# Performance work log

Measured on AMD Instinct MI355X. Metric: run time of the kernel, lower is better.

Reference implementation:

```python
import jax, jax.numpy as jnp
import numpy as np
import math

W_BITS = 256.0  # default w_bits in forward()

def ste_round(x):
    # straight-through estimator round: identity gradient
    return x + jax.lax.stop_gradient(jnp.round(x) - x)

def setup_inputs() -> dict:
    key = jax.random.key(0)
    k1, k2 = jax.random.split(key)
    x_size, y_size = 4096, 4096
    xb = jax.random.normal(k1, (8192, x_size), dtype=jnp.float32)
    W = jax.random.normal(k2, (x_size, y_size), dtype=jnp.float32) / math.sqrt(x_size)
    b = jnp.zeros((y_size,), dtype=jnp.float32)
    return {"xb": xb, "W": W, "b": b}

def reference(xb, W, b):
    # train=True path: fake-quant the weights (per-tensor symmetric int8), then matmul + bias
    s_w = 2.0 * jnp.max(jnp.abs(W)) / W_BITS          # per-tensor scale (zero-point 0)
    w_q = jnp.clip(ste_round(W / s_w), -127.0, 127.0)  # quantize + clamp
    w_fq = s_w * w_q                                    # dequantize (fake-quant)
    return xb @ w_fq + b
```

## Files before the change

### kernel.cpp

```cpp
#include <hip/hip_runtime.h>
#include <hip/hip_bf16.h>
#include <stdint.h>

typedef unsigned short u16;
typedef unsigned int u32;
typedef __bf16 bf16x8 __attribute__((ext_vector_type(8)));
typedef float f32x4 __attribute__((ext_vector_type(4)));
typedef u16 u16x4 __attribute__((ext_vector_type(4)));

typedef const __attribute__((address_space(1))) void* gas_ptr;
typedef __attribute__((address_space(3))) void* las_ptr;

#define M_DIM 8192
#define K_DIM 4096
#define N_DIM 4096

__device__ __forceinline__ u16 f32_to_bf16_rne(float f) {
    u32 u = __float_as_uint(f);
    u += 0x7FFFu + ((u >> 16) & 1u);
    return (u16)(u >> 16);
}

__global__ void maxabs_kernel(const float* __restrict__ W, u32* __restrict__ out, int n4) {
    int idx = blockIdx.x * blockDim.x + threadIdx.x;
    int stride = gridDim.x * blockDim.x;
    const float4* W4 = (const float4*)W;
    float m = 0.0f;
    for (int i = idx; i < n4; i += stride) {
        float4 v = W4[i];
        m = fmaxf(m, fmaxf(fmaxf(fabsf(v.x), fabsf(v.y)), fmaxf(fabsf(v.z), fabsf(v.w))));
    }
#pragma unroll
    for (int off = 32; off > 0; off >>= 1)
        m = fmaxf(m, __shfl_down(m, off));
    if ((threadIdx.x & 63) == 0)
        atomicMax(out, __float_as_uint(m));
}

__global__ void quant_transpose_kernel(const float* __restrict__ W, u16* __restrict__ Wt,
                                       const u32* __restrict__ mb) {
    __shared__ u16 tile[32][33];
    const float s_inv = 128.0f / __uint_as_float(*mb);
    int n = blockIdx.x * 32 + threadIdx.x;
#pragma unroll
    for (int r = threadIdx.y; r < 32; r += 8) {
        int k = blockIdx.y * 32 + r;
        float q = rintf(W[(size_t)k * N_DIM + n] * s_inv);
        q = fminf(fmaxf(q, -127.0f), 127.0f);
        tile[threadIdx.x][r] = (u16)(__float_as_uint(q) >> 16);
    }
    __syncthreads();
    int k_out = blockIdx.y * 32 + threadIdx.x;
#pragma unroll
    for (int r = threadIdx.y; r < 32; r += 8) {
        int n_out = blockIdx.x * 32 + r;
        Wt[(size_t)n_out * K_DIM + k_out] = tile[r][threadIdx.x];
    }
}

__global__ void cast_bf16_kernel(const float* __restrict__ x, u16* __restrict__ y, int n4) {
    int idx = blockIdx.x * blockDim.x + threadIdx.x;
    int stride = gridDim.x * blockDim.x;
    const float4* x4 = (const float4*)x;
    u16x4* y4 = (u16x4*)y;
    for (int i = idx; i < n4; i += stride) {
        float4 v = x4[i];
        u16x4 o;
        o.x = f32_to_bf16_rne(v.x);
        o.y = f32_to_bf16_rne(v.y);
        o.z = f32_to_bf16_rne(v.z);
        o.w = f32_to_bf16_rne(v.w);
        y4[i] = o;
    }
}


#define BAR() __builtin_amdgcn_s_barrier()
#define LGKM0()                                            \
    do {                                                   \
        asm volatile("s_waitcnt lgkmcnt(0)" ::: "memory"); \
        __builtin_amdgcn_sched_barrier(0);                 \
    } while (0)
#define VMC(N) asm volatile("s_waitcnt vmcnt(" #N ")" ::: "memory")
#define PRIO1() __builtin_amdgcn_s_setprio(1)
#define PRIO0() __builtin_amdgcn_s_setprio(0)

#define DS_A(ABASE, MH)                                            \
    do {                                                           \
        _Pragma("unroll") for (int i_ = 0; i_ < 4; ++i_) {         \
            const char* p_ = (ABASE) + ((MH)*64 + i_ * 16) * 128;  \
            a[i_][0] = *(const bf16x8*)(p_ + ck0);                 \
            a[i_][1] = *(const bf16x8*)(p_ + ck1);                 \
        }                                                          \
    } while (0)

#define DS_B(BBASE, NH)                                            \
    do {                                                           \
        _Pragma("unroll") for (int j_ = 0; j_ < 2; ++j_) {         \
            const char* p_ = (BBASE) + ((NH)*32 + j_ * 16) * 128;  \
            b[(NH)*2 + j_][0] = *(const bf16x8*)(p_ + ck0);        \
            b[(NH)*2 + j_][1] = *(const bf16x8*)(p_ + ck1);        \
        }                                                          \
    } while (0)

#define MM(MH, NH)                                                                            \
    do {                                                                                      \
        _Pragma("unroll") for (int i_ = 0; i_ < 4; ++i_) {                                    \
            _Pragma("unroll") for (int j_ = 0; j_ < 2; ++j_) {                                \
                f32x4& c_ = acc[(MH)*4 + i_][(NH)*2 + j_];                                    \
                c_ = __builtin_amdgcn_mfma_f32_16x16x32_bf16(a[i_][0], b[(NH)*2 + j_][0], c_, \
                                                             0, 0, 0);                        \
                c_ = __builtin_amdgcn_mfma_f32_16x16x32_bf16(a[i_][1], b[(NH)*2 + j_][1], c_, \
                                                             0, 0, 0);                        \
            }                                                                                 \
        }                                                                                     \
    } while (0)

#define STAGE_A(BUF, T, HALF)                                                                 \
    do {                                                                                      \
        const int r0_ = wave * 8 + (HALF)*64;                                                 \
        const u16* s_ = Ag + (size_t)r0_ * K_DIM + (T)*64;                                    \
        __builtin_amdgcn_global_load_lds((gas_ptr)s_, (las_ptr)&lds[BUF][r0_ * 64], 16, 0,    \
                                         0);                                                  \
        __builtin_amdgcn_global_load_lds((gas_ptr)(s_ + (size_t)128 * K_DIM),                 \
                                         (las_ptr)&lds[BUF][(r0_ + 128) * 64], 16, 0, 0);     \
    } while (0)

#define STAGE_B(BUF, T, HALF)                                                                  \
    do {                                                                                       \
        const int r0_ = bw + (HALF)*32;                                                        \
        const u16* s_ = Bg + (size_t)r0_ * K_DIM + (T)*64;                                     \
        __builtin_amdgcn_global_load_lds((gas_ptr)s_, (las_ptr)&lds[2 + (BUF)][r0_ * 64], 16,  \
                                         0, 0);                                                \
        __builtin_amdgcn_global_load_lds((gas_ptr)(s_ + (size_t)128 * K_DIM),                  \
                                         (las_ptr)&lds[2 + (BUF)][(r0_ + 128) * 64], 16, 0,    \
                                         0);                                                   \
    } while (0)

#define TILE(ABASE, BBASE, BUF, PBUF, T)            \
    do {                                            \
        DS_A(ABASE, 0);                             \
        DS_B(BBASE, 0);                             \
        STAGE_A(PBUF, (T) + 1, 1);                  \
        BAR();                                      \
        LGKM0();                                    \
        PRIO1();                                    \
        MM(0, 0);                                   \
        PRIO0();                                    \
        BAR();                                      \
        DS_B(BBASE, 1);                             \
        STAGE_B(PBUF, (T) + 1, 1);                  \
        BAR();                                      \
        LGKM0();                                    \
        PRIO1();                                    \
        MM(0, 1);                                   \
        PRIO0();                                    \
        BAR();                                      \
        DS_A(ABASE, 1);                             \
        STAGE_A(BUF, (T) + 2, 0);                   \
        BAR();                                      \
        LGKM0();                                    \
        PRIO1();                                    \
        MM(1, 0);                                   \
        PRIO0();                                    \
        BAR();                                      \
        STAGE_B(BUF, (T) + 2, 0);                   \
        BAR();                                      \
        PRIO1();                                    \
        MM(1, 1);                                   \
        PRIO0();                                    \
        VMC(4);                                     \
        BAR();                                      \
    } while (0)

__global__ __launch_bounds__(512, 2) void gemm_kernel(const u16* __restrict__ A,
                                                      const u16* __restrict__ Bt,
                                                      const float* __restrict__ bias,
                                                      const u32* __restrict__ mb,
                                                      float* __restrict__ out) {
    extern __shared__ u16 lds_raw[];
    u16(*lds)[256 * 64] = reinterpret_cast<u16(*)[256 * 64]>(lds_raw);

    const int tid = threadIdx.x;
    const int wave = tid >> 6;
    const int lane = tid & 63;
    const int quad = lane >> 4;
    const int l15 = lane & 15;
    const int wm = wave >> 2;
    const int wn = wave & 3;

    const int bswz = (blockIdx.x & 7) * 64 + (blockIdx.x >> 3);
    const int m0 = (bswz >> 4) * 256;
    const int n0 = (bswz & 15) * 256;

    const int stg_row = lane >> 3;
    const int stg_col = ((lane & 7) ^ stg_row) * 8;
    const u16* Ag = A + (size_t)(m0 + stg_row) * K_DIM + stg_col;
    const u16* Bg = Bt + (size_t)(n0 + stg_row) * K_DIM + stg_col;
    const int bw = (wave & 3) * 8 + (wave >> 2) * 64;

    const int xorv = (l15 & 7) << 4;
    const int ck0 = (quad * 16) ^ xorv;
    const int ck1 = (64 + quad * 16) ^ xorv;

    const char* asb0 = (const char*)&lds[0][0] + wm * 16384 + l15 * 128;
    const char* asb1 = asb0 + 32768;
    const char* bsb0 = (const char*)&lds[2][0] + wn * 8192 + l15 * 128;
    const char* bsb1 = bsb0 + 32768;

    bf16x8 a[4][2];
    bf16x8 b[4][2];
    f32x4 acc[8][4];
#pragma unroll
    for (int i = 0; i < 8; i++)
#pragma unroll
        for (int j = 0; j < 4; j++) acc[i][j] = (f32x4){0.f, 0.f, 0.f, 0.f};

    STAGE_A(0, 0, 0);
    STAGE_A(0, 0, 1);
    STAGE_B(0, 0, 0);
    STAGE_B(0, 0, 1);
    STAGE_A(1, 1, 0);
    STAGE_B(1, 1, 0);
    VMC(4);
    BAR();

#pragma unroll 1
    for (int t = 0; t < 62; t += 2) {
        TILE(asb0, bsb0, 0, 1, t);
        TILE(asb1, bsb1, 1, 0, t + 1);
    }

    DS_A(asb0, 0);
    DS_B(bsb0, 0);
    STAGE_A(1, 63, 1);
    BAR();
    LGKM0();
    PRIO1();
    MM(0, 0);
    PRIO0();
    BAR();
    DS_B(bsb0, 1);
    STAGE_B(1, 63, 1);
    BAR();
    LGKM0();
    PRIO1();
    MM(0, 1);
    PRIO0();
    BAR();
    DS_A(asb0, 1);
    BAR();
    LGKM0();
    PRIO1();
    MM(1, 0);
    PRIO0();
    BAR();
    PRIO1();
    MM(1, 1);
    PRIO0();
    VMC(0);
    BAR();

    DS_A(asb1, 0);
    DS_B(bsb1, 0);
    BAR();
    LGKM0();
    PRIO1();
    MM(0, 0);
    PRIO0();
    BAR();
    DS_B(bsb1, 1);
    BAR();
    LGKM0();
    PRIO1();
    MM(0, 1);
    PRIO0();
    BAR();
    DS_A(asb1, 1);
    BAR();
    LGKM0();
    PRIO1();
    MM(1, 0);
    MM(1, 1);
    PRIO0();

    const float s_w = __uint_as_float(*mb) * (1.0f / 128.0f);
#pragma unroll
    for (int nj = 0; nj < 4; ++nj) {
        const int col = n0 + wn * 64 + nj * 16 + l15;
        const float bv = bias[col];
#pragma unroll
        for (int mi = 0; mi < 8; ++mi) {
            const int row = m0 + wm * 128 + mi * 16 + quad * 4;
            float* op = out + (size_t)row * N_DIM + col;
#pragma unroll
            for (int r = 0; r < 4; ++r) op[(size_t)r * N_DIM] = s_w * acc[mi][nj][r] + bv;
        }
    }
}

extern "C" void kernel_launch(void* const* d_in, const int* in_sizes, int n_in,
                              void* d_out, int out_size, void* d_ws, size_t ws_size,
                              hipStream_t stream) {
    const float* xb = (const float*)d_in[0];
    const float* W = (const float*)d_in[1];
    const float* b = (const float*)d_in[2];
    float* out = (float*)d_out;

    u32* mb = (u32*)d_ws;
    u16* xb_bf = (u16*)((char*)d_ws + 256);
    u16* wqt = (u16*)((char*)d_ws + 256 + (size_t)M_DIM * K_DIM * 2);

    hipMemsetAsync(d_ws, 0, 4, stream);
    maxabs_kernel<<<1024, 256, 0, stream>>>(W, mb, (K_DIM * N_DIM) / 4);
    quant_transpose_kernel<<<dim3(N_DIM / 32, K_DIM / 32), dim3(32, 8), 0, stream>>>(W, wqt, mb);
    cast_bf16_kernel<<<4096, 256, 0, stream>>>(xb, xb_bf, (M_DIM * K_DIM) / 4);
    gemm_kernel<<<dim3(512), dim3(512), 131072, stream>>>(xb_bf, wqt, b, mb, out);
}
```

Baseline: 535.7 us.

## Restructure GEMM main loop into two-phase K-tile pipeline with fewer barriers

Replaces the four-phase-per-tile schedule (with explicit lgkmcnt waits and extra barriers) with a two-phase schedule per K tile. Each phase waits on a vmcnt count, issues the next tile's global-to-LDS loads, reads LDS fragments, then runs two MFMA blocks back-to-back. The peeled epilogue is removed and the loop wraps around with a dummy prefetch of tile 0. This is meant to cut barrier and wait overhead and let more MFMA work overlap memory traffic. The cost is possible LDS read/write hazards from the changed ordering and some wasted loads at the end.

```diff
diff --git a/kernel.cpp b/kernel.cpp
--- a/kernel.cpp
+++ b/kernel.cpp
@@ -76,11 +76,7 @@
 
 
 #define BAR() __builtin_amdgcn_s_barrier()
-#define LGKM0()                                            \
-    do {                                                   \
-        asm volatile("s_waitcnt lgkmcnt(0)" ::: "memory"); \
-        __builtin_amdgcn_sched_barrier(0);                 \
-    } while (0)
+#define SCB() __builtin_amdgcn_sched_barrier(0)
 #define VMC(N) asm volatile("s_waitcnt vmcnt(" #N ")" ::: "memory")
 #define PRIO1() __builtin_amdgcn_s_setprio(1)
 #define PRIO0() __builtin_amdgcn_s_setprio(0)
@@ -137,40 +133,32 @@
                                          0);                                                   \
     } while (0)
 
-#define TILE(ABASE, BBASE, BUF, PBUF, T)            \
-    do {                                            \
-        DS_A(ABASE, 0);                             \
-        DS_B(BBASE, 0);                             \
-        STAGE_A(PBUF, (T) + 1, 1);                  \
-        BAR();                                      \
-        LGKM0();                                    \
-        PRIO1();                                    \
-        MM(0, 0);                                   \
-        PRIO0();                                    \
-        BAR();                                      \
-        DS_B(BBASE, 1);                             \
-        STAGE_B(PBUF, (T) + 1, 1);                  \
-        BAR();                                      \
-        LGKM0();                                    \
-        PRIO1();                                    \
-        MM(0, 1);                                   \
-        PRIO0();                                    \
-        BAR();                                      \
-        DS_A(ABASE, 1);                             \
-        STAGE_A(BUF, (T) + 2, 0);                   \
-        BAR();                                      \
-        LGKM0();                                    \
-        PRIO1();                                    \
-        MM(1, 0);                                   \
-        PRIO0();                                    \
-        BAR();                                      \
-        STAGE_B(BUF, (T) + 2, 0);                   \
-        BAR();                                      \
-        PRIO1();                                    \
-        MM(1, 1);                                   \
-        PRIO0();                                    \
-        VMC(4);                                     \
-        BAR();                                      \
+#define KTILE(ABASE, BBASE, OBUF, TS)  \
+    do {                               \
+        VMC(2);                        \
+        BAR();                         \
+        SCB();                         \
+        STAGE_A(OBUF, TS, 0);          \
+        STAGE_B(OBUF, TS, 0);          \
+        STAGE_B(OBUF, TS, 1);          \
+        DS_A(ABASE, 0);                \
+        DS_B(BBASE, 0);                \
+        DS_B(BBASE, 1);                \
+        SCB();                         \
+        PRIO1();                       \
+        MM(0, 0);                      \
+        MM(0, 1);                      \
+        PRIO0();                       \
+        VMC(6);                        \
+        BAR();                         \
+        SCB();                         \
+        STAGE_A(OBUF, TS, 1);          \
+        DS_A(ABASE, 1);                \
+        SCB();                         \
+        PRIO1();                       \
+        MM(1, 0);                      \
+        MM(1, 1);                      \
+        PRIO0();                       \
     } while (0)
 
 __global__ __launch_bounds__(512, 2) void gemm_kernel(const u16* __restrict__ A,
@@ -217,72 +205,16 @@
         for (int j = 0; j < 4; j++) acc[i][j] = (f32x4){0.f, 0.f, 0.f, 0.f};
 
     STAGE_A(0, 0, 0);
-    STAGE_A(0, 0, 1);
     STAGE_B(0, 0, 0);
     STAGE_B(0, 0, 1);
-    STAGE_A(1, 1, 0);
-    STAGE_B(1, 1, 0);
-    VMC(4);
-    BAR();
+    STAGE_A(0, 0, 1);
 
 #pragma unroll 1
-    for (int t = 0; t < 62; t += 2) {
-        TILE(asb0, bsb0, 0, 1, t);
-        TILE(asb1, bsb1, 1, 0, t + 1);
-    }
-
-    DS_A(asb0, 0);
-    DS_B(bsb0, 0);
-    STAGE_A(1, 63, 1);
-    BAR();
-    LGKM0();
-    PRIO1();
-    MM(0, 0);
-    PRIO0();
-    BAR();
-    DS_B(bsb0, 1);
-    STAGE_B(1, 63, 1);
-    BAR();
-    LGKM0();
-    PRIO1();
-    MM(0, 1);
-    PRIO0();
-    BAR();
-    DS_A(asb0, 1);
-    BAR();
-    LGKM0();
-    PRIO1();
-    MM(1, 0);
-    PRIO0();
-    BAR();
-    PRIO1();
-    MM(1, 1);
-    PRIO0();
+    for (int t = 0; t < 64; t += 2) {
+        KTILE(asb0, bsb0, 1, t + 1);
+        KTILE(asb1, bsb1, 0, (t + 2) & 63);
+    }
     VMC(0);
-    BAR();
-
-    DS_A(asb1, 0);
-    DS_B(bsb1, 0);
-    BAR();
-    LGKM0();
-    PRIO1();
-    MM(0, 0);
-    PRIO0();
-    BAR();
-    DS_B(bsb1, 1);
-    BAR();
-    LGKM0();
-    PRIO1();
-    MM(0, 1);
-    PRIO0();
-    BAR();
-    DS_A(asb1, 1);
-    BAR();
-    LGKM0();
-    PRIO1();
-    MM(1, 0);
-    MM(1, 1);
-    PRIO0();
 
     const float s_w = __uint_as_float(*mb) * (1.0f / 128.0f);
 #pragma unroll
```

After: 558.2 us. 1.04x slower.
